# Optimization experiments

Hardware: AMD Instinct MI355X
Metric: run time of the kernel (lower is better)

The kernel has to match this reference:

```python
import jax, jax.numpy as jnp
import numpy as np

B, T, CV, DIM = 1, 1024, 8, 2048
NH, HD, W = 32, 64, 8
BMM = NH * HD


def swa_transform(x, window):
    # x: (b, t, cv, d) -> (b, t, window*cv, d)
    # matches torch pad-front + unfold + transpose + reshape: window-major, char-minor
    b, t, cv, d = x.shape
    xp = jnp.pad(x, ((0, 0), (window - 1, 0), (0, 0), (0, 0)))
    wins = jnp.stack([xp[:, w:w + t] for w in range(window)], axis=2)  # (b,t,W,cv,d)
    return wins.reshape(b, t, window * cv, d)


def rope(x, freqs):
    # interleaved-pair RoPE (rotary_embedding_torch default, theta=10000)
    # x: (..., hd); freqs broadcastable against x[..., 0::2]
    cos, sin = jnp.cos(freqs), jnp.sin(freqs)
    x1, x2 = x[..., 0::2], x[..., 1::2]
    return jnp.stack([x1 * cos - x2 * sin, x1 * sin + x2 * cos], axis=-1).reshape(x.shape)


def setup_inputs() -> dict:
    key = jax.random.key(0)
    ks = jax.random.split(key, 6)
    s = 0.02
    return {
        "x": jax.random.normal(ks[0], (B, T, DIM), dtype=jnp.float32),
        "chars": jax.random.normal(ks[1], (B, T, CV, DIM), dtype=jnp.float32),
        "wq": jax.random.normal(ks[2], (BMM, DIM), dtype=jnp.float32) * s,
        "wk": jax.random.normal(ks[3], (BMM, DIM), dtype=jnp.float32) * s,
        "wv": jax.random.normal(ks[4], (BMM, DIM), dtype=jnp.float32) * s,
        "wo": jax.random.normal(ks[5], (DIM, BMM), dtype=jnp.float32) * s,
    }


def reference(x, chars, wq, wk, wv, wo):
    b, t = x.shape[0], x.shape[1]
    cv = chars.shape[2]
    wc = W * cv

    q = x @ wq.T                     # (b, t, BMM)
    k = chars @ wk.T                 # (b, t, cv, BMM)
    v = chars @ wv.T

    k = swa_transform(k, W)          # (b, t, W*cv, BMM)
    v = swa_transform(v, W)

    q = q.reshape(b, t, NH, HD).transpose(0, 2, 1, 3)          # (b, nh, t, hd)
    k = k.reshape(b, t, wc, NH, HD).transpose(0, 3, 1, 2, 4)   # (b, nh, t, wc, hd)
    v = v.reshape(b, t, wc, NH, HD).transpose(0, 3, 1, 2, 4)   # (b, nh, t, wc, hd)

    inv_freq = 1.0 / (10000.0 ** (jnp.arange(0, HD, 2, dtype=jnp.float32) / HD))
    freqs = jnp.arange(t, dtype=jnp.float32)[:, None] * inv_freq  # (t, hd/2)

    q = rope(q, freqs)                       # rotate over token axis (-2)
    k = rope(k, freqs[:, None, :])           # rotate over token axis (-3), broadcast over window

    scores = jnp.einsum('bhtd,bhtkd->bhtk', q, k) / np.float32(np.sqrt(HD))
    attn = jax.nn.softmax(scores, axis=-1)   # (b, nh, t, wc)
    out = jnp.einsum('bhtk,bhtkd->bhtd', attn, v)
    out = out.transpose(0, 2, 1, 3).reshape(b, t, NH * HD)
    return out @ wo.T
```

## Files before the change

kernel.cpp:

```cpp
#include <hip/hip_runtime.h>
#include <hip/hip_bf16.h>
#include <cstdint>
#include <cstddef>

static constexpr int kT   = 1024;
static constexpr int kCV  = 8;
static constexpr int kDim = 2048;
static constexpr int kNH  = 32;
static constexpr int kHD  = 64;
static constexpr int kW   = 8;
static constexpr int kK   = 2048;

using bf16_t = __hip_bfloat16;

typedef __attribute__((ext_vector_type(8))) __bf16 bf16x8;
typedef __attribute__((ext_vector_type(4))) float  f32x4;

__device__ __forceinline__ float bf_bits_to_f32(unsigned short u) {
    union { unsigned int i; float f; } c;
    c.i = ((unsigned int)u) << 16;
    return c.f;
}

struct CastArgs {
    const float* src[6];
    bf16_t*      dst[6];
    int          cum[7];
};

__global__ void cast_all(CastArgs a, int total_chunks) {
    const int c = blockIdx.x * blockDim.x + threadIdx.x;
    if (c >= total_chunks) return;
    int r = 0;
#pragma unroll
    for (int i = 1; i <= 5; ++i) r += (c >= a.cum[i]) ? 1 : 0;
    const int local = c - a.cum[r];
    const float* s = a.src[r] + (size_t)local * 8;
    bf16_t*      d = a.dst[r] + (size_t)local * 8;
    const float4 lo = *reinterpret_cast<const float4*>(s);
    const float4 hi = *reinterpret_cast<const float4*>(s + 4);
    union { bf16_t h[8]; uint4 u; } o;
    o.h[0] = __float2bfloat16(lo.x); o.h[1] = __float2bfloat16(lo.y);
    o.h[2] = __float2bfloat16(lo.z); o.h[3] = __float2bfloat16(lo.w);
    o.h[4] = __float2bfloat16(hi.x); o.h[5] = __float2bfloat16(hi.y);
    o.h[6] = __float2bfloat16(hi.z); o.h[7] = __float2bfloat16(hi.w);
    *reinterpret_cast<uint4*>(d) = o.u;
}

template <bool OUT_BF16, typename CT>
__device__ __forceinline__ void gemm_body(const bf16_t* __restrict__ A,
                                          const bf16_t* __restrict__ Wt,
                                          CT* __restrict__ C,
                                          int bm, int bn, int ldc) {
    __shared__ bf16_t As[128 * 64];
    __shared__ bf16_t Bs[128 * 64];

    const int tid  = threadIdx.x;
    const int wave = tid >> 6;
    const int lane = tid & 63;
    const int l16  = lane & 15;
    const int quad = lane >> 4;
    const int wm   = (wave >> 1) * 64;
    const int wn   = (wave & 1) * 64;

    f32x4 acc[4][4];
#pragma unroll
    for (int i = 0; i < 4; ++i)
#pragma unroll
        for (int j = 0; j < 4; ++j) acc[i][j] = (f32x4)0.0f;

    const int srow = tid >> 3;
    const int jg   = (tid & 7) ^ (srow & 7);
    const bf16_t* gA = A  + (size_t)(bm + srow) * kK + jg * 8;
    const bf16_t* gB = Wt + (size_t)(bn + srow) * kK + jg * 8;

    for (int k0 = 0; k0 < kK; k0 += 64) {
#pragma unroll
        for (int i = 0; i < 4; ++i) {
            __builtin_amdgcn_global_load_lds(
                (const __attribute__((address_space(1))) void*)(gA + (size_t)i * 32 * kK + k0),
                (__attribute__((address_space(3))) void*)(As + i * 2048 + wave * 512),
                16, 0, 0);
            __builtin_amdgcn_global_load_lds(
                (const __attribute__((address_space(1))) void*)(gB + (size_t)i * 32 * kK + k0),
                (__attribute__((address_space(3))) void*)(Bs + i * 2048 + wave * 512),
                16, 0, 0);
        }
        __syncthreads();

#pragma unroll
        for (int ph = 0; ph < 2; ++ph) {
            bf16x8 af[4], bfr[4];
#pragma unroll
            for (int i = 0; i < 4; ++i) {
                const int jla = (ph * 4 + quad) ^ (l16 & 7);
                af[i]  = *reinterpret_cast<const bf16x8*>(
                    &As[(wm + i * 16 + l16) * 64 + jla * 8]);
                bfr[i] = *reinterpret_cast<const bf16x8*>(
                    &Bs[(wn + i * 16 + l16) * 64 + jla * 8]);
            }
#pragma unroll
            for (int i = 0; i < 4; ++i)
#pragma unroll
                for (int j = 0; j < 4; ++j)
                    acc[i][j] = __builtin_amdgcn_mfma_f32_16x16x32_bf16(
                        af[i], bfr[j], acc[i][j], 0, 0, 0);
        }
        __syncthreads();
    }

#pragma unroll
    for (int i = 0; i < 4; ++i) {
#pragma unroll
        for (int rr = 0; rr < 4; ++rr) {
            const int row = bm + wm + i * 16 + quad * 4 + rr;
#pragma unroll
            for (int j = 0; j < 4; ++j) {
                const int col = bn + wn + j * 16 + l16;
                if constexpr (OUT_BF16) {
                    C[(size_t)row * ldc + col] = __float2bfloat16(acc[i][j][rr]);
                } else {
                    C[(size_t)row * ldc + col] = acc[i][j][rr];
                }
            }
        }
    }
}

__global__ __launch_bounds__(256, 3) void proj_kernel(
    const bf16_t* __restrict__ xb, const bf16_t* __restrict__ cb,
    const bf16_t* __restrict__ wqb, const bf16_t* __restrict__ wkvb,
    bf16_t* __restrict__ qb, bf16_t* __restrict__ kvb) {
    const int bid = blockIdx.x;
    if (bid < 2048) {
        const int bm = (bid >> 5) * 128;
        const int bn = (bid & 31) * 128;
        gemm_body<true>(cb, wkvb, kvb, bm, bn, 4096);
    } else {
        const int t  = bid - 2048;
        const int bm = (t >> 4) * 128;
        const int bn = (t & 15) * 128;
        gemm_body<true>(xb, wqb, qb, bm, bn, 2048);
    }
}

__global__ __launch_bounds__(256, 3) void out_gemm(
    const bf16_t* __restrict__ ob, const bf16_t* __restrict__ wob,
    float* __restrict__ out) {
    const int bm = (blockIdx.x >> 4) * 128;
    const int bn = (blockIdx.x & 15) * 128;
    gemm_body<false>(ob, wob, out, bm, bn, 2048);
}

static constexpr int kTT   = 16;
static constexpr int kSRC  = kTT + kW - 1;
static constexpr int kROWS = kSRC * kCV;
static constexpr int kLDK  = 72;

__global__ __launch_bounds__(1024) void attn_kernel(
    const bf16_t* __restrict__ qb,
    const bf16_t* __restrict__ kvb,
    bf16_t* __restrict__ ob) {
    __shared__ unsigned short kl[kROWS * kLDK];
    __shared__ unsigned short vl[kROWS * kLDK];
    __shared__ float ql[kTT * 64];
    __shared__ float al[kTT * 64];

    const int t0   = blockIdx.x * kTT;
    const int h    = blockIdx.y;
    const int tid  = threadIdx.x;
    const int wave = tid >> 6;
    const int lane = tid & 63;

    ql[tid] = __bfloat162float(qb[(size_t)(t0 + wave) * kDim + h * kHD + lane]);

    const long long grow0 = (long long)(t0 - (kW - 1)) * kCV;
#pragma unroll
    for (int c = tid; c < kROWS * 8; c += 1024) {
        const int r   = c >> 3;
        const int sub = c & 7;
        const long long grow = grow0 + r;
        uint4 kd = make_uint4(0, 0, 0, 0), vd = make_uint4(0, 0, 0, 0);
        if (grow >= 0) {
            const size_t gb = (size_t)grow * 4096 + h * kHD + sub * 8;
            kd = *reinterpret_cast<const uint4*>(kvb + gb);
            vd = *reinterpret_cast<const uint4*>(kvb + gb + 2048);
        }
        *reinterpret_cast<uint4*>(&kl[r * kLDK + sub * 8]) = kd;
        *reinterpret_cast<uint4*>(&vl[r * kLDK + sub * 8]) = vd;
    }
    __syncthreads();

    const int r = wave * kCV + lane;
    float s = 0.0f;
#pragma unroll
    for (int c = 0; c < 8; ++c) {
        union { uint4 u; unsigned short us[8]; } kv;
        kv.u = *reinterpret_cast<const uint4*>(&kl[r * kLDK + c * 8]);
        const float4 qa = *reinterpret_cast<const float4*>(&ql[wave * 64 + c * 8]);
        const float4 qc = *reinterpret_cast<const float4*>(&ql[wave * 64 + c * 8 + 4]);
        s += bf_bits_to_f32(kv.us[0]) * qa.x + bf_bits_to_f32(kv.us[1]) * qa.y +
             bf_bits_to_f32(kv.us[2]) * qa.z + bf_bits_to_f32(kv.us[3]) * qa.w +
             bf_bits_to_f32(kv.us[4]) * qc.x + bf_bits_to_f32(kv.us[5]) * qc.y +
             bf_bits_to_f32(kv.us[6]) * qc.z + bf_bits_to_f32(kv.us[7]) * qc.w;
    }
    s *= 0.125f;

    float m = s;
#pragma unroll
    for (int off = 32; off; off >>= 1) m = fmaxf(m, __shfl_xor(m, off));
    const float e = __expf(s - m);
    float sum = e;
#pragma unroll
    for (int off = 32; off; off >>= 1) sum += __shfl_xor(sum, off);
    al[wave * 64 + lane] = e / sum;

    float o = 0.0f;
#pragma unroll
    for (int k2 = 0; k2 < 64; ++k2)
        o += al[wave * 64 + k2] * bf_bits_to_f32(vl[(wave * kCV + k2) * kLDK + lane]);
    ob[(size_t)(t0 + wave) * kDim + h * kHD + lane] = __float2bfloat16(o);
}

extern "C" void kernel_launch(void* const* d_in, const int* in_sizes, int n_in,
                              void* d_out, int out_size, void* d_ws,
                              size_t ws_size, hipStream_t stream) {
    const float* x     = (const float*)d_in[0];
    const float* chars = (const float*)d_in[1];
    const float* wq    = (const float*)d_in[2];
    const float* wk    = (const float*)d_in[3];
    const float* wv    = (const float*)d_in[4];
    const float* wo    = (const float*)d_in[5];
    float* out = (float*)d_out;

    char* p = (char*)d_ws;
    bf16_t* xb   = (bf16_t*)p; p += (size_t)kT * kDim * 2;
    bf16_t* cb   = (bf16_t*)p; p += (size_t)kT * kCV * kDim * 2;
    bf16_t* wqb  = (bf16_t*)p; p += (size_t)kDim * kDim * 2;
    bf16_t* wkvb = (bf16_t*)p; p += (size_t)2 * kDim * kDim * 2;
    bf16_t* wob  = (bf16_t*)p; p += (size_t)kDim * kDim * 2;
    bf16_t* qb   = (bf16_t*)p; p += (size_t)kT * kDim * 2;
    bf16_t* kvb  = (bf16_t*)p; p += (size_t)kT * kCV * 2 * kDim * 2;
    bf16_t* ob   = (bf16_t*)p; p += (size_t)kT * kDim * 2;

    CastArgs ca;
    ca.src[0] = x;     ca.dst[0] = xb;
    ca.src[1] = chars; ca.dst[1] = cb;
    ca.src[2] = wq;    ca.dst[2] = wqb;
    ca.src[3] = wk;    ca.dst[3] = wkvb;
    ca.src[4] = wv;    ca.dst[4] = wkvb + (size_t)kDim * kDim;
    ca.src[5] = wo;    ca.dst[5] = wob;
    const int sizes[6] = {kT * kDim, kT * kCV * kDim, kDim * kDim,
                          kDim * kDim, kDim * kDim, kDim * kDim};
    int cum = 0;
    ca.cum[0] = 0;
    for (int i = 0; i < 6; ++i) { cum += sizes[i] / 8; ca.cum[i + 1] = cum; }
    cast_all<<<dim3((cum + 255) / 256), dim3(256), 0, stream>>>(ca, cum);

    proj_kernel<<<dim3(2176), dim3(256), 0, stream>>>(xb, cb, wqb, wkvb, qb, kvb);

    attn_kernel<<<dim3(kT / kTT, kNH), dim3(1024), 0, stream>>>(qb, kvb, ob);

    out_gemm<<<dim3(128), dim3(256), 0, stream>>>(ob, wob, out);
}
```

Before: 357.2 us.

## Use 256x256 double-buffered projection GEMM and split-K output GEMM

Replaces the 128x128 single-buffered projection GEMM with a 256x256 tile kernel of 512 threads. It uses 128KB of dynamic LDS as two buffers and overlaps the global-to-LDS load of tile k+2 with the MFMAs on the current tile, raising setprio around the compute. The output GEMM is split over K into two halves that accumulate with fp32 atomicAdd into a zeroed output, doubling block count from 128 to 256 so more CUs are busy. This adds a memset, makes the result order nondeterministic, and the large tiles limit occupancy.

```diff
diff --git a/kernel.cpp b/kernel.cpp
--- a/kernel.cpp
+++ b/kernel.cpp
@@ -47,11 +47,142 @@
     *reinterpret_cast<uint4*>(d) = o.u;
 }
 
-template <bool OUT_BF16, typename CT>
-__device__ __forceinline__ void gemm_body(const bf16_t* __restrict__ A,
-                                          const bf16_t* __restrict__ Wt,
-                                          CT* __restrict__ C,
-                                          int bm, int bn, int ldc) {
+__device__ __forceinline__ void gemm256_body(const bf16_t* __restrict__ A,
+                                             const bf16_t* __restrict__ Wt,
+                                             bf16_t* __restrict__ C,
+                                             int bm, int bn, int ldc,
+                                             bf16_t* smem) {
+    const int tid  = threadIdx.x;
+    const int wave = tid >> 6;
+    const int lane = tid & 63;
+    const int l16  = lane & 15;
+    const int quad = lane >> 4;
+    const int wm   = (wave >> 2) * 128;
+    const int wn   = (wave & 3) * 64;
+
+    f32x4 acc[8][4];
+#pragma unroll
+    for (int i = 0; i < 8; ++i)
+#pragma unroll
+        for (int j = 0; j < 4; ++j) acc[i][j] = (f32x4)0.0f;
+
+    const int srow = tid >> 3;
+    const int jg   = (tid & 7) ^ (srow & 7);
+    const bf16_t* gA = A  + (size_t)(bm + srow) * kK + jg * 8;
+    const bf16_t* gB = Wt + (size_t)(bn + srow) * kK + jg * 8;
+    const int ldsw = wave * 512;
+
+    auto stage = [&](int kt, int p) {
+        const int k0 = kt * 64;
+        bf16_t* As = smem + p * 32768;
+        bf16_t* Bs = As + 16384;
+#pragma unroll
+        for (int i = 0; i < 4; ++i)
+            __builtin_amdgcn_global_load_lds(
+                (const __attribute__((address_space(1))) void*)(gA + (size_t)i * 64 * kK + k0),
+                (__attribute__((address_space(3))) void*)(As + i * 4096 + ldsw),
+                16, 0, 0);
+#pragma unroll
+        for (int i = 0; i < 4; ++i)
+            __builtin_amdgcn_global_load_lds(
+                (const __attribute__((address_space(1))) void*)(gB + (size_t)i * 64 * kK + k0),
+                (__attribute__((address_space(3))) void*)(Bs + i * 4096 + ldsw),
+                16, 0, 0);
+    };
+
+    bf16x8 af[8], bq[4];
+    auto rdfrags = [&](int p, int ph) {
+        const bf16_t* As = smem + p * 32768;
+        const bf16_t* Bs = As + 16384;
+        const int jla = (ph * 4 + quad) ^ (l16 & 7);
+#pragma unroll
+        for (int i = 0; i < 8; ++i)
+            af[i] = *reinterpret_cast<const bf16x8*>(
+                &As[(wm + i * 16 + l16) * 64 + jla * 8]);
+#pragma unroll
+        for (int j = 0; j < 4; ++j)
+            bq[j] = *reinterpret_cast<const bf16x8*>(
+                &Bs[(wn + j * 16 + l16) * 64 + jla * 8]);
+    };
+    auto domfma = [&]() {
+#pragma unroll
+        for (int i = 0; i < 8; ++i)
+#pragma unroll
+            for (int j = 0; j < 4; ++j)
+                acc[i][j] = __builtin_amdgcn_mfma_f32_16x16x32_bf16(
+                    af[i], bq[j], acc[i][j], 0, 0, 0);
+    };
+
+    stage(0, 0);
+    stage(1, 1);
+    asm volatile("s_waitcnt vmcnt(8)" ::: "memory");
+    __builtin_amdgcn_s_barrier();
+
+    static_assert(kK / 64 == 32, "NT");
+    int p = 0;
+    for (int t = 0; t < 30; ++t) {
+        rdfrags(p, 0);
+        domfma();
+        rdfrags(p, 1);
+        asm volatile("s_waitcnt lgkmcnt(0)" ::: "memory");
+        __builtin_amdgcn_s_barrier();
+        stage(t + 2, p);
+        __builtin_amdgcn_s_setprio(1);
+        domfma();
+        __builtin_amdgcn_s_setprio(0);
+        asm volatile("s_waitcnt vmcnt(8)" ::: "memory");
+        __builtin_amdgcn_s_barrier();
+        p ^= 1;
+    }
+    rdfrags(p, 0); domfma();
+    rdfrags(p, 1);
+    __builtin_amdgcn_s_setprio(1);
+    domfma();
+    __builtin_amdgcn_s_setprio(0);
+    asm volatile("s_waitcnt vmcnt(0)" ::: "memory");
+    __builtin_amdgcn_s_barrier();
+    p ^= 1;
+    rdfrags(p, 0); domfma();
+    rdfrags(p, 1); domfma();
+
+#pragma unroll
+    for (int i = 0; i < 8; ++i) {
+#pragma unroll
+        for (int rr = 0; rr < 4; ++rr) {
+            const int row = bm + wm + i * 16 + quad * 4 + rr;
+#pragma unroll
+            for (int j = 0; j < 4; ++j) {
+                const int col = bn + wn + j * 16 + l16;
+                C[(size_t)row * ldc + col] = __float2bfloat16(acc[i][j][rr]);
+            }
+        }
+    }
+}
+
+__global__ __launch_bounds__(512, 2) void proj256_kernel(
+    const bf16_t* __restrict__ xb, const bf16_t* __restrict__ cb,
+    const bf16_t* __restrict__ wqb, const bf16_t* __restrict__ wkvb,
+    bf16_t* __restrict__ qb, bf16_t* __restrict__ kvb) {
+    extern __shared__ bf16_t smem[];
+    const int bid = blockIdx.x;
+    if (bid < 512) {
+        const int bm = (bid >> 4) * 256;
+        const int bn = (bid & 15) * 256;
+        gemm256_body(cb, wkvb, kvb, bm, bn, 4096, smem);
+    } else {
+        const int t  = bid - 512;
+        const int bm = (t >> 3) * 256;
+        const int bn = (t & 7) * 256;
+        gemm256_body(xb, wqb, qb, bm, bn, 2048, smem);
+    }
+}
+
+template <bool ATOMIC>
+__device__ __forceinline__ void gemm_body128(const bf16_t* __restrict__ A,
+                                             const bf16_t* __restrict__ Wt,
+                                             float* __restrict__ C,
+                                             int bm, int bn, int ldc,
+                                             int kbeg, int kend) {
     __shared__ bf16_t As[128 * 64];
     __shared__ bf16_t Bs[128 * 64];
 
@@ -70,11 +201,11 @@
         for (int j = 0; j < 4; ++j) acc[i][j] = (f32x4)0.0f;
 
     const int srow = tid >> 3;
-    const int jg   = (tid & 7) ^ (srow & 7);
-    const bf16_t* gA = A  + (size_t)(bm + srow) * kK + jg * 8;
-    const bf16_t* gB = Wt + (size_t)(bn + srow) * kK + jg * 8;
-
-    for (int k0 = 0; k0 < kK; k0 += 64) {
+    const int jgs  = (tid & 7) ^ (srow & 7);
+    const bf16_t* gA = A  + (size_t)(bm + srow) * kK + jgs * 8;
+    const bf16_t* gB = Wt + (size_t)(bn + srow) * kK + jgs * 8;
+
+    for (int k0 = kbeg; k0 < kend; k0 += 64) {
 #pragma unroll
         for (int i = 0; i < 4; ++i) {
             __builtin_amdgcn_global_load_lds(
@@ -117,8 +248,8 @@
 #pragma unroll
             for (int j = 0; j < 4; ++j) {
                 const int col = bn + wn + j * 16 + l16;
-                if constexpr (OUT_BF16) {
-                    C[(size_t)row * ldc + col] = __float2bfloat16(acc[i][j][rr]);
+                if constexpr (ATOMIC) {
+                    atomicAdd(&C[(size_t)row * ldc + col], acc[i][j][rr]);
                 } else {
                     C[(size_t)row * ldc + col] = acc[i][j][rr];
                 }
@@ -127,29 +258,14 @@
     }
 }
 
-__global__ __launch_bounds__(256, 3) void proj_kernel(
-    const bf16_t* __restrict__ xb, const bf16_t* __restrict__ cb,
-    const bf16_t* __restrict__ wqb, const bf16_t* __restrict__ wkvb,
-    bf16_t* __restrict__ qb, bf16_t* __restrict__ kvb) {
-    const int bid = blockIdx.x;
-    if (bid < 2048) {
-        const int bm = (bid >> 5) * 128;
-        const int bn = (bid & 31) * 128;
-        gemm_body<true>(cb, wkvb, kvb, bm, bn, 4096);
-    } else {
-        const int t  = bid - 2048;
-        const int bm = (t >> 4) * 128;
-        const int bn = (t & 15) * 128;
-        gemm_body<true>(xb, wqb, qb, bm, bn, 2048);
-    }
-}
-
 __global__ __launch_bounds__(256, 3) void out_gemm(
     const bf16_t* __restrict__ ob, const bf16_t* __restrict__ wob,
     float* __restrict__ out) {
-    const int bm = (blockIdx.x >> 4) * 128;
-    const int bn = (blockIdx.x & 15) * 128;
-    gemm_body<false>(ob, wob, out, bm, bn, 2048);
+    const int tile = blockIdx.x & 127;
+    const int ks   = blockIdx.x >> 7;
+    const int bm = (tile >> 4) * 128;
+    const int bn = (tile & 15) * 128;
+    gemm_body128<true>(ob, wob, out, bm, bn, 2048, ks * 1024, ks * 1024 + 1024);
 }
 
 static constexpr int kTT   = 16;
@@ -242,6 +358,15 @@
     bf16_t* qb   = (bf16_t*)p; p += (size_t)kT * kDim * 2;
     bf16_t* kvb  = (bf16_t*)p; p += (size_t)kT * kCV * 2 * kDim * 2;
     bf16_t* ob   = (bf16_t*)p; p += (size_t)kT * kDim * 2;
+
+    static int attr_done = 0;
+    if (!attr_done) {
+        hipFuncSetAttribute(reinterpret_cast<const void*>(proj256_kernel),
+                            hipFuncAttributeMaxDynamicSharedMemorySize, 131072);
+        attr_done = 1;
+    }
+
+    hipMemsetAsync(out, 0, (size_t)kT * kDim * sizeof(float), stream);
 
     CastArgs ca;
     ca.src[0] = x;     ca.dst[0] = xb;
@@ -257,9 +382,10 @@
     for (int i = 0; i < 6; ++i) { cum += sizes[i] / 8; ca.cum[i + 1] = cum; }
     cast_all<<<dim3((cum + 255) / 256), dim3(256), 0, stream>>>(ca, cum);
 
-    proj_kernel<<<dim3(2176), dim3(256), 0, stream>>>(xb, cb, wqb, wkvb, qb, kvb);
+    proj256_kernel<<<dim3(544), dim3(512), 131072, stream>>>(
+        xb, cb, wqb, wkvb, qb, kvb);
 
     attn_kernel<<<dim3(kT / kTT, kNH), dim3(1024), 0, stream>>>(qb, kvb, ob);
 
-    out_gemm<<<dim3(128), dim3(256), 0, stream>>>(ob, wob, out);
-}
+    out_gemm<<<dim3(256), dim3(256), 0, stream>>>(ob, wob, out);
+}
```

After: 386.8 us. +8.3%, slower.

## Use 128x64 tiles for output GEMM, split attention PV accumulators, retune launch bounds

Applied to the files above, without the earlier changes.

The output projection GEMM now uses its own 128x64 tile kernel with a 256-block grid instead of 128 blocks of 128x128, so more of the GPU's compute units get work for this small GEMM. The attention PV reduction is split into four independent accumulators to shorten the dependent FMA chain. The occupancy hint for the projection kernel is raised from 3 to 4 blocks per CU, which may constrain register allocation and cause spills.

```diff
diff --git a/kernel.cpp b/kernel.cpp
--- a/kernel.cpp
+++ b/kernel.cpp
@@ -127,7 +127,7 @@
     }
 }
 
-__global__ __launch_bounds__(256, 3) void proj_kernel(
+__global__ __launch_bounds__(256, 4) void proj_kernel(
     const bf16_t* __restrict__ xb, const bf16_t* __restrict__ cb,
     const bf16_t* __restrict__ wqb, const bf16_t* __restrict__ wkvb,
     bf16_t* __restrict__ qb, bf16_t* __restrict__ kvb) {
@@ -144,12 +144,83 @@
     }
 }
 
-__global__ __launch_bounds__(256, 3) void out_gemm(
+__global__ __launch_bounds__(256, 2) void out_gemm(
     const bf16_t* __restrict__ ob, const bf16_t* __restrict__ wob,
     float* __restrict__ out) {
-    const int bm = (blockIdx.x >> 4) * 128;
-    const int bn = (blockIdx.x & 15) * 128;
-    gemm_body<false>(ob, wob, out, bm, bn, 2048);
+    __shared__ bf16_t As[128 * 64];
+    __shared__ bf16_t Bs[64 * 64];
+
+    const int bm = (blockIdx.x >> 5) * 128;
+    const int bn = (blockIdx.x & 31) * 64;
+
+    const int tid  = threadIdx.x;
+    const int wave = tid >> 6;
+    const int lane = tid & 63;
+    const int l16  = lane & 15;
+    const int quad = lane >> 4;
+    const int wm   = (wave >> 1) * 64;
+    const int wn   = (wave & 1) * 32;
+
+    f32x4 acc[4][2];
+#pragma unroll
+    for (int i = 0; i < 4; ++i)
+#pragma unroll
+        for (int j = 0; j < 2; ++j) acc[i][j] = (f32x4)0.0f;
+
+    const int srow = tid >> 3;
+    const int jg   = (tid & 7) ^ (srow & 7);
+    const bf16_t* gA = ob  + (size_t)(bm + srow) * kK + jg * 8;
+    const bf16_t* gB = wob + (size_t)(bn + srow) * kK + jg * 8;
+
+    for (int k0 = 0; k0 < kK; k0 += 64) {
+#pragma unroll
+        for (int i = 0; i < 4; ++i)
+            __builtin_amdgcn_global_load_lds(
+                (const __attribute__((address_space(1))) void*)(gA + (size_t)i * 32 * kK + k0),
+                (__attribute__((address_space(3))) void*)(As + i * 2048 + wave * 512),
+                16, 0, 0);
+#pragma unroll
+        for (int i = 0; i < 2; ++i)
+            __builtin_amdgcn_global_load_lds(
+                (const __attribute__((address_space(1))) void*)(gB + (size_t)i * 32 * kK + k0),
+                (__attribute__((address_space(3))) void*)(Bs + i * 2048 + wave * 512),
+                16, 0, 0);
+        __syncthreads();
+
+#pragma unroll
+        for (int ph = 0; ph < 2; ++ph) {
+            const int jla = (ph * 4 + quad) ^ (l16 & 7);
+            bf16x8 af[4], bfr[2];
+#pragma unroll
+            for (int i = 0; i < 4; ++i)
+                af[i] = *reinterpret_cast<const bf16x8*>(
+                    &As[(wm + i * 16 + l16) * 64 + jla * 8]);
+#pragma unroll
+            for (int j = 0; j < 2; ++j)
+                bfr[j] = *reinterpret_cast<const bf16x8*>(
+                    &Bs[(wn + j * 16 + l16) * 64 + jla * 8]);
+#pragma unroll
+            for (int i = 0; i < 4; ++i)
+#pragma unroll
+                for (int j = 0; j < 2; ++j)
+                    acc[i][j] = __builtin_amdgcn_mfma_f32_16x16x32_bf16(
+                        af[i], bfr[j], acc[i][j], 0, 0, 0);
+        }
+        __syncthreads();
+    }
+
+#pragma unroll
+    for (int i = 0; i < 4; ++i) {
+#pragma unroll
+        for (int rr = 0; rr < 4; ++rr) {
+            const int row = bm + wm + i * 16 + quad * 4 + rr;
+#pragma unroll
+            for (int j = 0; j < 2; ++j) {
+                const int col = bn + wn + j * 16 + l16;
+                out[(size_t)row * 2048 + col] = acc[i][j][rr];
+            }
+        }
+    }
 }
 
 static constexpr int kTT   = 16;
@@ -215,10 +286,19 @@
     for (int off = 32; off; off >>= 1) sum += __shfl_xor(sum, off);
     al[wave * 64 + lane] = e / sum;
 
-    float o = 0.0f;
-#pragma unroll
-    for (int k2 = 0; k2 < 64; ++k2)
-        o += al[wave * 64 + k2] * bf_bits_to_f32(vl[(wave * kCV + k2) * kLDK + lane]);
+    float o0 = 0.0f, o1 = 0.0f, o2 = 0.0f, o3 = 0.0f;
+#pragma unroll
+    for (int k2 = 0; k2 < 64; k2 += 4) {
+        o0 += al[wave * 64 + k2 + 0] *
+              bf_bits_to_f32(vl[(wave * kCV + k2 + 0) * kLDK + lane]);
+        o1 += al[wave * 64 + k2 + 1] *
+              bf_bits_to_f32(vl[(wave * kCV + k2 + 1) * kLDK + lane]);
+        o2 += al[wave * 64 + k2 + 2] *
+              bf_bits_to_f32(vl[(wave * kCV + k2 + 2) * kLDK + lane]);
+        o3 += al[wave * 64 + k2 + 3] *
+              bf_bits_to_f32(vl[(wave * kCV + k2 + 3) * kLDK + lane]);
+    }
+    const float o = (o0 + o1) + (o2 + o3);
     ob[(size_t)(t0 + wave) * kDim + h * kHD + lane] = __float2bfloat16(o);
 }
 
@@ -261,5 +341,5 @@
 
     attn_kernel<<<dim3(kT / kTT, kNH), dim3(1024), 0, stream>>>(qb, kvb, ob);
 
-    out_gemm<<<dim3(128), dim3(256), 0, stream>>>(ob, wob, out);
-}
+    out_gemm<<<dim3(256), dim3(256), 0, stream>>>(ob, wob, out);
+}
```

Measured after the change: 370.3 us. 1.04x slower.
